# Performance work log

Hardware: AMD Instinct MI355X
Metric: run time of the kernel (lower is better)

Reference implementation:

```python
import jax, jax.numpy as jnp
import numpy as np
from jax import lax

HEADS, DIM_HEAD, LANDMARKS, PINV_ITERS = 8, 64, 256, 6
D = 512


def layernorm(x, w, b, eps=1e-5):
    mu = x.mean(-1, keepdims=True)
    var = ((x - mu) ** 2).mean(-1, keepdims=True)
    return (x - mu) * lax.rsqrt(var + eps) * w + b


def pinv_iter(x, iters=PINV_ITERS):
    # Moore-Penrose pseudo-inverse via Newton-Schulz (lucidrains nystrom-attention)
    abs_x = jnp.abs(x)
    z = jnp.swapaxes(x, -1, -2) / (jnp.max(abs_x.sum(-1)) * jnp.max(abs_x.sum(-2)))
    I = jnp.eye(x.shape[-1], dtype=x.dtype)
    for _ in range(iters):
        xz = x @ z
        z = 0.25 * z @ (13 * I - xz @ (15 * I - xz @ (7 * I - xz)))
    return z


def nystrom_attention(x, qkv_w, out_w, out_b, res_w):
    b, n, _ = x.shape
    m = LANDMARKS
    pad = (m - n % m) % m
    xp = jnp.pad(x, ((0, 0), (pad, 0), (0, 0)))  # left-pad seq to multiple of m
    n_p = n + pad
    q, k, v = jnp.split(xp @ qkv_w, 3, axis=-1)
    split = lambda t: t.reshape(b, n_p, HEADS, DIM_HEAD).transpose(0, 2, 1, 3)
    q, k, v = split(q), split(k), split(v)  # (b, h, n_p, d)
    q = q * DIM_HEAD ** -0.5
    l = n_p // m  # tokens per landmark
    q_l = q.reshape(b, HEADS, m, l, DIM_HEAD).mean(3)  # (b, h, m, d)
    k_l = k.reshape(b, HEADS, m, l, DIM_HEAD).mean(3)
    a1 = jax.nn.softmax(jnp.einsum('bhnd,bhmd->bhnm', q, k_l), -1)  # (b,h,n_p,m)
    a2 = jax.nn.softmax(jnp.einsum('bhmd,bhld->bhml', q_l, k_l), -1)  # (b,h,m,m)
    a3 = jax.nn.softmax(jnp.einsum('bhmd,bhnd->bhmn', q_l, k), -1)  # (b,h,m,n_p)
    out = (a1 @ pinv_iter(a2)) @ (a3 @ v)  # (b,h,n_p,d)
    # depthwise residual conv over the seq dim, kernel (33,1), one per head
    res = lax.conv_general_dilated(v, res_w, (1, 1), [(16, 16), (0, 0)],
                                   dimension_numbers=('NCHW', 'OIHW', 'NCHW'),
                                   feature_group_count=HEADS)
    out = out + res
    out = out.transpose(0, 2, 1, 3).reshape(b, n_p, HEADS * DIM_HEAD)
    return (out @ out_w + out_b)[:, -n:]


def ppeg(x, Hh, Ww, w7, b7, w5, b5, w3, b3):
    B, _, C = x.shape
    cls_tok, feat = x[:, :1], x[:, 1:]
    f = feat.transpose(0, 2, 1).reshape(B, C, Hh, Ww)
    def dwconv(w, bb, p):
        return lax.conv_general_dilated(f, w, (1, 1), [(p, p), (p, p)],
                                        dimension_numbers=('NCHW', 'OIHW', 'NCHW'),
                                        feature_group_count=C) + bb[None, :, None, None]
    y = f + dwconv(w7, b7, 3) + dwconv(w5, b5, 2) + dwconv(w3, b3, 1)
    y = y.reshape(B, C, Hh * Ww).transpose(0, 2, 1)
    return jnp.concatenate([cls_tok, y], axis=1)


def setup_inputs() -> dict:
    key = jax.random.key(0)
    ks = jax.random.split(key, 16)
    E, NC, H = 1024, 4, HEADS
    f32 = jnp.float32
    rn = lambda k, shp, s=0.02: (jax.random.normal(k, shp, f32) * s)
    return {
        'x': jax.random.normal(ks[0], (1, 40960, E), f32),
        'fc1_w': rn(ks[1], (E, D)), 'fc1_b': jnp.zeros((D,), f32),
        'cls_token': jax.random.normal(ks[2], (1, 1, D), f32),
        'l1_norm_w': jnp.ones((D,), f32), 'l1_norm_b': jnp.zeros((D,), f32),
        'l1_qkv_w': rn(ks[3], (D, 3 * D)),
        'l1_out_w': rn(ks[4], (D, D)), 'l1_out_b': jnp.zeros((D,), f32),
        'l1_res_w': rn(ks[5], (H, 1, 33, 1), 0.1),
        'ppeg_w7': rn(ks[6], (D, 1, 7, 7), 0.1), 'ppeg_b7': jnp.zeros((D,), f32),
        'ppeg_w5': rn(ks[7], (D, 1, 5, 5), 0.1), 'ppeg_b5': jnp.zeros((D,), f32),
        'ppeg_w3': rn(ks[8], (D, 1, 3, 3), 0.1), 'ppeg_b3': jnp.zeros((D,), f32),
        'l2_norm_w': jnp.ones((D,), f32), 'l2_norm_b': jnp.zeros((D,), f32),
        'l2_qkv_w': rn(ks[9], (D, 3 * D)),
        'l2_out_w': rn(ks[10], (D, D)), 'l2_out_b': jnp.zeros((D,), f32),
        'l2_res_w': rn(ks[11], (H, 1, 33, 1), 0.1),
        'norm_w': jnp.ones((D,), f32), 'norm_b': jnp.zeros((D,), f32),
        'fc3_w': rn(ks[12], (D, NC)), 'fc3_b': jnp.zeros((NC,), f32),
    }


def reference(x, fc1_w, fc1_b, cls_token, l1_norm_w, l1_norm_b, l1_qkv_w, l1_out_w, l1_out_b, l1_res_w, ppeg_w7, ppeg_b7, ppeg_w5, ppeg_b5, ppeg_w3, ppeg_b3, l2_norm_w, l2_norm_b, l2_qkv_w, l2_out_w, l2_out_b, l2_res_w, norm_w, norm_b, fc3_w, fc3_b):
    B, N, E = x.shape  # (1, 40960, 1024)
    POOL_OUT = 20480
    # AdaptiveMaxPool2d((20480, E)) on a (1, N, E) tensor: max-pool seq dim N -> 20480
    ft = x.reshape(B, POOL_OUT, N // POOL_OUT, E).max(axis=2)
    ft = jax.nn.relu(ft @ fc1_w + fc1_b)  # (1, 20480, 512)
    Hn = ft.shape[1]
    _H = int(np.ceil(np.sqrt(Hn)))  # 144
    add = _H * _H - Hn  # 256
    ft = jnp.concatenate([ft, ft[:, :add]], axis=1)  # (1, 20736, 512)
    h = jnp.concatenate([jnp.broadcast_to(cls_token, (B, 1, D)), ft], axis=1)  # 20737 tokens
    h = h + nystrom_attention(layernorm(h, l1_norm_w, l1_norm_b), l1_qkv_w, l1_out_w, l1_out_b, l1_res_w)
    h = ppeg(h, _H, _H, ppeg_w7, ppeg_b7, ppeg_w5, ppeg_b5, ppeg_w3, ppeg_b3)
    h = h + nystrom_attention(layernorm(h, l2_norm_w, l2_norm_b), l2_qkv_w, l2_out_w, l2_out_b, l2_res_w)
    h = layernorm(h, norm_w, norm_b)[:, 0]
    logits = h @ fc3_w + fc3_b
    return logits, jax.nn.softmax(logits, -1), jnp.argmax(logits, -1)
```

## Files before the change

### kernel.cpp

```cpp
#include <hip/hip_runtime.h>


constexpr int D_    = 512;
constexpr int E_    = 1024;
constexpr int NTOK  = 20737;
constexpr int NP_   = 20992;
constexpr int NH_   = 8;
constexpr int HD_   = 64;
constexpr int MLM   = 256;
constexpr int LCH   = 82;
constexpr int HHW   = 144;
constexpr int NFEAT = 20736;
constexpr int PADR  = 255;
constexpr int NCH   = 41;
constexpr int CHTOK = 512;

typedef __attribute__((ext_vector_type(8))) short bf16x8;
typedef __attribute__((ext_vector_type(4))) float f32x4;

__device__ __forceinline__ unsigned short f2bf(float f){
  unsigned int u = __float_as_uint(f);
  unsigned int r = u + 0x7fffu + ((u >> 16) & 1u);
  return (unsigned short)(r >> 16);
}
__device__ __forceinline__ float bfu(unsigned short u){
  return __uint_as_float((unsigned int)u << 16);
}

__device__ __forceinline__ float waveMaxF(float v){
#pragma unroll
  for (int o = 32; o > 0; o >>= 1) v = fmaxf(v, __shfl_xor(v, o));
  return v;
}
__device__ __forceinline__ float waveSumF(float v){
#pragma unroll
  for (int o = 32; o > 0; o >>= 1) v += __shfl_xor(v, o);
  return v;
}
__device__ __forceinline__ float blockMax256(float v, float* sbuf){
  v = waveMaxF(v);
  if ((threadIdx.x & 63) == 0) sbuf[threadIdx.x >> 6] = v;
  __syncthreads();
  float r = fmaxf(fmaxf(sbuf[0], sbuf[1]), fmaxf(sbuf[2], sbuf[3]));
  __syncthreads();
  return r;
}
__device__ __forceinline__ float blockSum256(float v, float* sbuf){
  v = waveSumF(v);
  if ((threadIdx.x & 63) == 0) sbuf[threadIdx.x >> 6] = v;
  __syncthreads();
  float r = sbuf[0] + sbuf[1] + sbuf[2] + sbuf[3];
  __syncthreads();
  return r;
}

__global__ __launch_bounds__(256) void wtrans_kernel(
    const float* __restrict__ W, unsigned short* __restrict__ Wt, int K, int N){
  __shared__ float tile[32][33];
  const int kb = blockIdx.x * 32, nb = blockIdx.y * 32;
  const int tx = threadIdx.x, ty = threadIdx.y;
  for (int i = ty; i < 32; i += 8) tile[i][tx] = W[(size_t)(kb + i) * N + nb + tx];
  __syncthreads();
  for (int i = ty; i < 32; i += 8)
    Wt[(size_t)(nb + i) * K + kb + tx] = f2bf(tile[tx][i]);
}

__global__ __launch_bounds__(256) void pool_bf16_kernel(
    const float* __restrict__ x, unsigned short* __restrict__ Ah){
  size_t idx4 = ((size_t)blockIdx.x * 256 + threadIdx.x) * 4;
  size_t m = idx4 >> 10, e = idx4 & 1023;
  float4 a = *(const float4*)(x + (m * 2) * E_ + e);
  float4 b = *(const float4*)(x + (m * 2 + 1) * E_ + e);
  unsigned long long pk =
      (unsigned long long)f2bf(fmaxf(a.x, b.x))
    | ((unsigned long long)f2bf(fmaxf(a.y, b.y)) << 16)
    | ((unsigned long long)f2bf(fmaxf(a.z, b.z)) << 32)
    | ((unsigned long long)f2bf(fmaxf(a.w, b.w)) << 48);
  *(unsigned long long*)(Ah + idx4) = pk;
}

__device__ __forceinline__ void mfma_tile64(
    const unsigned short* __restrict__ A, int arows, int bm,
    const unsigned short* __restrict__ Bt, int bn, int K,
    f32x4 acc[2][2], unsigned short* As, unsigned short* Bs){
  const int t = threadIdx.x;
  const int lane = t & 63, wave = t >> 6;
  const int wr = wave >> 1, wc = wave & 1;
  const int m16 = lane & 15, quad = lane >> 4;
  for (int kc = 0; kc < K; kc += 64){
    for (int idx = t; idx < 512; idx += 256){
      int row = idx >> 3, off = (idx & 7) * 8;
      int ga = bm + row;
      ulonglong2 av = {0ull, 0ull};
      if (ga < arows) av = *(const ulonglong2*)(A + (size_t)ga * K + kc + off);
      *(ulonglong2*)(As + row * 72 + off) = av;
      ulonglong2 bv = *(const ulonglong2*)(Bt + (size_t)(bn + row) * K + kc + off);
      *(ulonglong2*)(Bs + row * 72 + off) = bv;
    }
    __syncthreads();
#pragma unroll
    for (int k2 = 0; k2 < 64; k2 += 32){
      bf16x8 a0 = *(const bf16x8*)(As + (wr * 32 + m16) * 72 + k2 + quad * 8);
      bf16x8 a1 = *(const bf16x8*)(As + (wr * 32 + 16 + m16) * 72 + k2 + quad * 8);
      bf16x8 b0 = *(const bf16x8*)(Bs + (wc * 32 + m16) * 72 + k2 + quad * 8);
      bf16x8 b1 = *(const bf16x8*)(Bs + (wc * 32 + 16 + m16) * 72 + k2 + quad * 8);
      acc[0][0] = __builtin_amdgcn_mfma_f32_16x16x32_bf16(a0, b0, acc[0][0], 0, 0, 0);
      acc[0][1] = __builtin_amdgcn_mfma_f32_16x16x32_bf16(a0, b1, acc[0][1], 0, 0, 0);
      acc[1][0] = __builtin_amdgcn_mfma_f32_16x16x32_bf16(a1, b0, acc[1][0], 0, 0, 0);
      acc[1][1] = __builtin_amdgcn_mfma_f32_16x16x32_bf16(a1, b1, acc[1][1], 0, 0, 0);
    }
    __syncthreads();
  }
}

__global__ __launch_bounds__(256) void fc1_mfma_kernel(
    const unsigned short* __restrict__ Ah, const unsigned short* __restrict__ Bt,
    const float* __restrict__ bias, float* __restrict__ h){
  __shared__ unsigned short As[64 * 72], Bs[64 * 72];
  f32x4 z4 = {0.f, 0.f, 0.f, 0.f};
  f32x4 acc[2][2] = {{z4, z4}, {z4, z4}};
  const int bm = blockIdx.x * 64, bn = blockIdx.y * 64;
  mfma_tile64(Ah, 20480, bm, Bt, bn, E_, acc, As, Bs);
  const int lane = threadIdx.x & 63, wave = threadIdx.x >> 6;
  const int wr = wave >> 1, wc = wave & 1;
  const int m16 = lane & 15, quad = lane >> 4;
#pragma unroll
  for (int mi = 0; mi < 2; mi++)
#pragma unroll
    for (int ni = 0; ni < 2; ni++){
      int col = bn + wc * 32 + ni * 16 + m16;
      float bv = bias[col];
#pragma unroll
      for (int r = 0; r < 4; r++){
        int row = bm + wr * 32 + mi * 16 + quad * 4 + r;
        float vv = fmaxf(acc[mi][ni][r] + bv, 0.f);
        h[(size_t)(1 + row) * D_ + col] = vv;
        if (row < 256) h[(size_t)(20481 + row) * D_ + col] = vv;
      }
    }
}

__global__ void cls_kernel(const float* __restrict__ cls, float* __restrict__ h){
  int c = blockIdx.x * 256 + threadIdx.x;
  if (c < D_) h[c] = cls[c];
}

__global__ __launch_bounds__(256) void ln_pad_kernel(
    const float* __restrict__ h, const float* __restrict__ w,
    const float* __restrict__ b, unsigned short* __restrict__ xph){
  const int r = blockIdx.x;
  const int t = threadIdx.x;
  if (r < PADR){
    xph[(size_t)r * D_ + t] = 0;
    xph[(size_t)r * D_ + 256 + t] = 0;
    return;
  }
  __shared__ float s4[4];
  const float* x = h + (size_t)(r - PADR) * D_;
  float a0 = x[t], a1 = x[t + 256];
  float mu = blockSum256(a0 + a1, s4) * (1.f / 512.f);
  float d0 = a0 - mu, d1 = a1 - mu;
  float var = blockSum256(d0 * d0 + d1 * d1, s4) * (1.f / 512.f);
  float rs = rsqrtf(var + 1e-5f);
  xph[(size_t)r * D_ + t]       = f2bf(d0 * rs * w[t] + b[t]);
  xph[(size_t)r * D_ + 256 + t] = f2bf(d1 * rs * w[t + 256] + b[t + 256]);
}

__global__ __launch_bounds__(256) void qkv_mfma_kernel(
    const unsigned short* __restrict__ A, const unsigned short* __restrict__ Bt,
    unsigned short* __restrict__ q16, unsigned short* __restrict__ k16,
    unsigned short* __restrict__ v16){
  __shared__ unsigned short As[64 * 72], Bs[64 * 72];
  f32x4 z4 = {0.f, 0.f, 0.f, 0.f};
  f32x4 acc[2][2] = {{z4, z4}, {z4, z4}};
  const int bm = blockIdx.x * 64, bn = blockIdx.y * 64;
  mfma_tile64(A, NP_, bm, Bt, bn, D_, acc, As, Bs);
  const int lane = threadIdx.x & 63, wave = threadIdx.x >> 6;
  const int wr = wave >> 1, wc = wave & 1;
  const int m16 = lane & 15, quad = lane >> 4;
#pragma unroll
  for (int mi = 0; mi < 2; mi++)
#pragma unroll
    for (int ni = 0; ni < 2; ni++){
      int col = bn + wc * 32 + ni * 16 + m16;
      int which = col >> 9, hh = (col >> 6) & 7, d = col & 63;
      size_t cbase = (size_t)hh * NP_ * HD_ + d;
      unsigned short* dst;
      float sc = 1.f;
      if (which == 0){ dst = q16; sc = 0.125f; }
      else if (which == 1) dst = k16;
      else dst = v16;
#pragma unroll
      for (int r = 0; r < 4; r++){
        int row = bm + wr * 32 + mi * 16 + quad * 4 + r;
        dst[cbase + (size_t)row * HD_] = f2bf(acc[mi][ni][r] * sc);
      }
    }
}

__global__ __launch_bounds__(64) void landmark_kernel(
    const unsigned short* __restrict__ q16, const unsigned short* __restrict__ k16,
    float* __restrict__ ql, float* __restrict__ kl,
    unsigned short* __restrict__ qlh, unsigned short* __restrict__ klh){
  const int im = blockIdx.x, h = blockIdx.y, d = threadIdx.x;
  size_t base = ((size_t)h * NP_ + (size_t)im * LCH) * HD_ + d;
  float sq = 0.f, sk = 0.f;
  for (int r = 0; r < LCH; r++){
    sq += bfu(q16[base + (size_t)r * HD_]);
    sk += bfu(k16[base + (size_t)r * HD_]);
  }
  float qm = sq * (1.f / 82.f), km = sk * (1.f / 82.f);
  size_t oidx = ((size_t)h * MLM + im) * HD_ + d;
  ql[oidx] = qm;  qlh[oidx] = f2bf(qm);
  kl[oidx] = km;  klh[oidx] = f2bf(km);
}

__global__ __launch_bounds__(256) void a2_kernel(
    const float* __restrict__ ql, const float* __restrict__ kl,
    float* __restrict__ a2){
  const int im = blockIdx.x, h = blockIdx.y, t = threadIdx.x;
  __shared__ __align__(16) float qs[64];
  __shared__ float s4[4];
  if (t < 64) qs[t] = ql[((size_t)h * MLM + im) * HD_ + t];
  __syncthreads();
  const float4* kr4 = (const float4*)(kl + ((size_t)h * MLM + t) * HD_);
  const float4* qs4 = (const float4*)qs;
  float s = 0.f;
#pragma unroll
  for (int d4 = 0; d4 < 16; d4++){
    float4 kv = kr4[d4], qv = qs4[d4];
    s += qv.x*kv.x + qv.y*kv.y + qv.z*kv.z + qv.w*kv.w;
  }
  float mx = blockMax256(s, s4);
  float e = __expf(s - mx);
  float S = blockSum256(e, s4);
  a2[((size_t)h * MLM + im) * MLM + t] = e / S;
}

__global__ __launch_bounds__(256) void pinv_scale_kernel(
    const float* __restrict__ a2, float* __restrict__ scal){
  const int h = blockIdx.x, j = threadIdx.x;
  const float* A = a2 + (size_t)h * MLM * MLM;
  float rs = 0.f, cs = 0.f;
  for (int t = 0; t < MLM; t++){
    rs += fabsf(A[(size_t)j * MLM + t]);
    cs += fabsf(A[(size_t)t * MLM + j]);
  }
  __shared__ float s4[4];
  float rmax = blockMax256(rs, s4);
  float cmax = blockMax256(cs, s4);
  if (j == 0){ scal[h * 2] = rmax; scal[h * 2 + 1] = cmax; }
}

__global__ __launch_bounds__(256) void pinv_init_kernel(
    const float* __restrict__ a2, const float* __restrict__ scal,
    float* __restrict__ z){
  const int i = blockIdx.x, h = blockIdx.y, j = threadIdx.x;
  float rmax = scal[0], cmax = scal[1];
#pragma unroll
  for (int hh = 1; hh < 8; hh++){
    rmax = fmaxf(rmax, scal[hh * 2]);
    cmax = fmaxf(cmax, scal[hh * 2 + 1]);
  }
  float inv = 1.f / (rmax * cmax);
  z[((size_t)h * MLM + i) * MLM + j] = a2[((size_t)h * MLM + j) * MLM + i] * inv;
}

__global__ __launch_bounds__(256) void bmm256_mfma_kernel(
    const float* __restrict__ Ab, const float* __restrict__ Bb,
    float* __restrict__ Cb, float c0, float sgn, float c1){
  __shared__ unsigned short Ash[64 * 40], Asl[64 * 40];
  __shared__ unsigned short Bsh[64 * 40], Bsl[64 * 40];
  const int h = blockIdx.z;
  const float* A = Ab + (size_t)h * 65536;
  const float* B = Bb + (size_t)h * 65536;
  float* C = Cb + (size_t)h * 65536;
  const int bm = blockIdx.x * 64, bn = blockIdx.y * 64;
  const int t = threadIdx.x, lane = t & 63, w = t >> 6;
  const int wr = w >> 1, wc = w & 1, m16 = lane & 15, quad = lane >> 4;
  f32x4 z4 = {0.f, 0.f, 0.f, 0.f};
  f32x4 acc[2][2] = {{z4, z4}, {z4, z4}};
  for (int kc = 0; kc < 256; kc += 32){
    {
      int row = t >> 2, c8 = (t & 3) * 8;
      const float* src = A + (size_t)(bm + row) * 256 + kc + c8;
      float xs[8];
      *(float4*)(xs)     = *(const float4*)src;
      *(float4*)(xs + 4) = *(const float4*)(src + 4);
#pragma unroll
      for (int j = 0; j < 8; j++){
        unsigned short hi = f2bf(xs[j]);
        Ash[row * 40 + c8 + j] = hi;
        Asl[row * 40 + c8 + j] = f2bf(xs[j] - bfu(hi));
      }
      int k = t >> 3, n8 = (t & 7) * 8;
      const float* bsrc = B + (size_t)(kc + k) * 256 + bn + n8;
      float ys[8];
      *(float4*)(ys)     = *(const float4*)bsrc;
      *(float4*)(ys + 4) = *(const float4*)(bsrc + 4);
#pragma unroll
      for (int j = 0; j < 8; j++){
        float xv = sgn * ys[j];
        if (kc + k == bn + n8 + j) xv += c0;
        unsigned short hi = f2bf(xv);
        Bsh[(n8 + j) * 40 + k] = hi;
        Bsl[(n8 + j) * 40 + k] = f2bf(xv - bfu(hi));
      }
    }
    __syncthreads();
    bf16x8 ah[2], al[2], bh[2], bl[2];
#pragma unroll
    for (int mi = 0; mi < 2; mi++){
      ah[mi] = *(const bf16x8*)(Ash + (wr * 32 + mi * 16 + m16) * 40 + quad * 8);
      al[mi] = *(const bf16x8*)(Asl + (wr * 32 + mi * 16 + m16) * 40 + quad * 8);
      bh[mi] = *(const bf16x8*)(Bsh + (wc * 32 + mi * 16 + m16) * 40 + quad * 8);
      bl[mi] = *(const bf16x8*)(Bsl + (wc * 32 + mi * 16 + m16) * 40 + quad * 8);
    }
#pragma unroll
    for (int mi = 0; mi < 2; mi++)
#pragma unroll
      for (int ni = 0; ni < 2; ni++){
        acc[mi][ni] = __builtin_amdgcn_mfma_f32_16x16x32_bf16(ah[mi], bh[ni], acc[mi][ni], 0, 0, 0);
        acc[mi][ni] = __builtin_amdgcn_mfma_f32_16x16x32_bf16(ah[mi], bl[ni], acc[mi][ni], 0, 0, 0);
        acc[mi][ni] = __builtin_amdgcn_mfma_f32_16x16x32_bf16(al[mi], bh[ni], acc[mi][ni], 0, 0, 0);
      }
    __syncthreads();
  }
#pragma unroll
  for (int mi = 0; mi < 2; mi++)
#pragma unroll
    for (int ni = 0; ni < 2; ni++)
#pragma unroll
      for (int r = 0; r < 4; r++){
        int row = bm + wr * 32 + mi * 16 + quad * 4 + r;
        int col = bn + wc * 32 + ni * 16 + m16;
        C[(size_t)row * 256 + col] = c1 * acc[mi][ni][r];
      }
}

__global__ __launch_bounds__(256) void a3v_part_kernel(
    const unsigned short* __restrict__ qlh, const unsigned short* __restrict__ k16,
    const unsigned short* __restrict__ v16, float* __restrict__ pacc,
    float* __restrict__ pml){
  __shared__ __align__(16) unsigned short qs16[64 * 72];
  __shared__ __align__(16) unsigned short kb16[64 * 72];
  __shared__ __align__(16) unsigned short vt16[64 * 72];
  const int lt = blockIdx.x, h = blockIdx.y, ch = blockIdx.z;
  const int t = threadIdx.x;
  const int lane = t & 63, w = t >> 6;
  const int m16 = lane & 15, quad = lane >> 4;

  const unsigned short* qg = qlh + ((size_t)h * MLM + lt * 64) * HD_;
  for (int idx = t; idx < 512; idx += 256){
    int row = idx >> 3, off = (idx & 7) * 8;
    *(uint4*)(qs16 + row * 72 + off) = *(const uint4*)(qg + (size_t)row * HD_ + off);
  }
  f32x4 z4 = {0.f, 0.f, 0.f, 0.f};
  f32x4 acc_o[4] = {z4, z4, z4, z4};
  float mreg[4], lreg[4];
#pragma unroll
  for (int r = 0; r < 4; r++){ mreg[r] = -3.0e38f; lreg[r] = 0.f; }
  const unsigned short* kg = k16 + ((size_t)h * NP_ + ch * CHTOK) * HD_;
  const unsigned short* vg = v16 + ((size_t)h * NP_ + ch * CHTOK) * HD_;

  for (int sc = 0; sc < 8; sc++){
    __syncthreads();
    for (int idx = t; idx < 512; idx += 256){
      int row = idx >> 3, off = (idx & 7) * 8;
      *(uint4*)(kb16 + row * 72 + off) =
          *(const uint4*)(kg + (size_t)(sc * 64 + row) * HD_ + off);
      uint4 pv = *(const uint4*)(vg + (size_t)(sc * 64 + row) * HD_ + off);
      unsigned int uu[4] = {pv.x, pv.y, pv.z, pv.w};
#pragma unroll
      for (int j = 0; j < 4; j++){
        vt16[(off + 2 * j)     * 72 + row] = (unsigned short)(uu[j] & 0xffffu);
        vt16[(off + 2 * j + 1) * 72 + row] = (unsigned short)(uu[j] >> 16);
      }
    }
    __syncthreads();
    f32x4 acc_s[4] = {z4, z4, z4, z4};
#pragma unroll
    for (int kc = 0; kc < 64; kc += 32){
      bf16x8 a = *(const bf16x8*)(qs16 + (w * 16 + m16) * 72 + kc + quad * 8);
#pragma unroll
      for (int ni = 0; ni < 4; ni++){
        bf16x8 b = *(const bf16x8*)(kb16 + (ni * 16 + m16) * 72 + kc + quad * 8);
        acc_s[ni] = __builtin_amdgcn_mfma_f32_16x16x32_bf16(a, b, acc_s[ni], 0, 0, 0);
      }
    }
    __syncthreads();
#pragma unroll
    for (int r = 0; r < 4; r++){
      float cm = fmaxf(fmaxf(acc_s[0][r], acc_s[1][r]), fmaxf(acc_s[2][r], acc_s[3][r]));
#pragma unroll
      for (int o = 1; o < 16; o <<= 1) cm = fmaxf(cm, __shfl_xor(cm, o));
      float mn = fmaxf(mreg[r], cm);
      float scl = __expf(mreg[r] - mn);
      float p0 = __expf(acc_s[0][r] - mn), p1 = __expf(acc_s[1][r] - mn);
      float p2 = __expf(acc_s[2][r] - mn), p3 = __expf(acc_s[3][r] - mn);
      float ls = (p0 + p1) + (p2 + p3);
#pragma unroll
      for (int o = 1; o < 16; o <<= 1) ls += __shfl_xor(ls, o);
      lreg[r] = lreg[r] * scl + ls;
      mreg[r] = mn;
      acc_o[0][r] *= scl; acc_o[1][r] *= scl;
      acc_o[2][r] *= scl; acc_o[3][r] *= scl;
      int prow = (w * 16 + quad * 4 + r) * 72 + m16;
      kb16[prow + 0]  = f2bf(p0);
      kb16[prow + 16] = f2bf(p1);
      kb16[prow + 32] = f2bf(p2);
      kb16[prow + 48] = f2bf(p3);
    }
    __syncthreads();
#pragma unroll
    for (int kc = 0; kc < 64; kc += 32){
      bf16x8 a = *(const bf16x8*)(kb16 + (w * 16 + m16) * 72 + kc + quad * 8);
#pragma unroll
      for (int ni = 0; ni < 4; ni++){
        bf16x8 b = *(const bf16x8*)(vt16 + (ni * 16 + m16) * 72 + kc + quad * 8);
        acc_o[ni] = __builtin_amdgcn_mfma_f32_16x16x32_bf16(a, b, acc_o[ni], 0, 0, 0);
      }
    }
  }
#pragma unroll
  for (int r = 0; r < 4; r++){
    int im = lt * 64 + w * 16 + quad * 4 + r;
    size_t base = ((size_t)h * NCH + ch) * MLM + im;
#pragma unroll
    for (int ni = 0; ni < 4; ni++)
      pacc[base * HD_ + ni * 16 + m16] = acc_o[ni][r];
    if (m16 == 0){
      pml[base * 2]     = mreg[r];
      pml[base * 2 + 1] = lreg[r];
    }
  }
}

__global__ __launch_bounds__(64) void a3v_combine_kernel(
    const float* __restrict__ pacc, const float* __restrict__ pml,
    float* __restrict__ t1){
  const int im = blockIdx.x, h = blockIdx.y, lane = threadIdx.x;
  float M = -3.0e38f;
  for (int c = 0; c < NCH; c++)
    M = fmaxf(M, pml[(((size_t)h * NCH + c) * MLM + im) * 2]);
  float accv = 0.f, L = 0.f;
  for (int c = 0; c < NCH; c++){
    size_t base = ((size_t)h * NCH + c) * MLM + im;
    float mc = pml[base * 2], lc = pml[base * 2 + 1];
    float w = __expf(mc - M);
    accv += w * pacc[base * HD_ + lane];
    L += w * lc;
  }
  t1[((size_t)h * MLM + im) * HD_ + lane] = accv / L;
}

__global__ __launch_bounds__(256) void zt1_kernel(
    const float* __restrict__ z, const float* __restrict__ t1,
    unsigned short* __restrict__ t2t){
  const int h = blockIdx.y;
  const int t = threadIdx.x;
  const int d = t & 63, ri = t >> 6;
  const int im = blockIdx.x * 4 + ri;
  const float* zr = z + ((size_t)h * MLM + im) * MLM;
  const float* t1h = t1 + (size_t)h * MLM * HD_;
  float acc = 0.f;
#pragma unroll 8
  for (int kk = 0; kk < MLM; kk++) acc += zr[kk] * t1h[(size_t)kk * HD_ + d];
  t2t[((size_t)h * HD_ + d) * MLM + im] = f2bf(acc);
}

__global__ __launch_bounds__(256) void out_tile_kernel(
    const unsigned short* __restrict__ q16, const unsigned short* __restrict__ klh,
    const unsigned short* __restrict__ t2t, const unsigned short* __restrict__ v16,
    const float* __restrict__ resw, unsigned short* __restrict__ outh){
  __shared__ __align__(16) unsigned short smem[64 * 72 * 2 + 64 * 264];
  unsigned short* qs16 = smem;
  unsigned short* kb16 = smem + 64 * 72;
  unsigned short* Ps   = smem + 64 * 72 * 2;
  const int tile = blockIdx.x, h = blockIdx.y;
  const int n0 = PADR + tile * 64;
  const int t = threadIdx.x;
  const int lane = t & 63, w = t >> 6;
  const int m16 = lane & 15, quad = lane >> 4;

  {
    const unsigned short* qh = q16 + (size_t)h * NP_ * HD_;
    for (int idx = t; idx < 512; idx += 256){
      int row = idx >> 3, off = (idx & 7) * 8;
      int n = n0 + row;
      uint4 val = {0u, 0u, 0u, 0u};
      if (n < NP_) val = *(const uint4*)(qh + (size_t)n * HD_ + off);
      *(uint4*)(qs16 + row * 72 + off) = val;
    }
  }
  f32x4 z4 = {0.f, 0.f, 0.f, 0.f};
  f32x4 acc_s[16];
#pragma unroll
  for (int i = 0; i < 16; i++) acc_s[i] = z4;
  const unsigned short* klg = klh + (size_t)h * MLM * HD_;
  for (int m = 0; m < 4; m++){
    __syncthreads();
    for (int idx = t; idx < 512; idx += 256){
      int row = idx >> 3, off = (idx & 7) * 8;
      *(uint4*)(kb16 + row * 72 + off) =
          *(const uint4*)(klg + (size_t)(m * 64 + row) * HD_ + off);
    }
    __syncthreads();
#pragma unroll
    for (int kc = 0; kc < 64; kc += 32){
      bf16x8 a = *(const bf16x8*)(qs16 + (w * 16 + m16) * 72 + kc + quad * 8);
#pragma unroll
      for (int ni = 0; ni < 4; ni++){
        bf16x8 b = *(const bf16x8*)(kb16 + (ni * 16 + m16) * 72 + kc + quad * 8);
        acc_s[m * 4 + ni] = __builtin_amdgcn_mfma_f32_16x16x32_bf16(a, b, acc_s[m * 4 + ni], 0, 0, 0);
      }
    }
  }
  __syncthreads();
#pragma unroll
  for (int r = 0; r < 4; r++){
    float mx = acc_s[0][r];
#pragma unroll
    for (int mc = 1; mc < 16; mc++) mx = fmaxf(mx, acc_s[mc][r]);
#pragma unroll
    for (int o = 1; o < 16; o <<= 1) mx = fmaxf(mx, __shfl_xor(mx, o));
    float p[16]; float sum = 0.f;
#pragma unroll
    for (int mc = 0; mc < 16; mc++){ p[mc] = __expf(acc_s[mc][r] - mx); sum += p[mc]; }
#pragma unroll
    for (int o = 1; o < 16; o <<= 1) sum += __shfl_xor(sum, o);
    float inv = 1.f / sum;
    int prow = (w * 16 + quad * 4 + r) * 264;
#pragma unroll
    for (int mc = 0; mc < 16; mc++)
      Ps[prow + (mc >> 2) * 64 + (mc & 3) * 16 + m16] = f2bf(p[mc] * inv);
  }
  f32x4 acc_o[4] = {z4, z4, z4, z4};
  const unsigned short* t2g = t2t + (size_t)h * HD_ * MLM;
  for (int ch = 0; ch < 4; ch++){
    __syncthreads();
    {
      int row = t >> 2, c8 = (t & 3) * 16;
      const unsigned short* src = t2g + (size_t)row * MLM + ch * 64 + c8;
      *(uint4*)(kb16 + row * 72 + c8)     = *(const uint4*)src;
      *(uint4*)(kb16 + row * 72 + c8 + 8) = *(const uint4*)(src + 8);
    }
    __syncthreads();
#pragma unroll
    for (int kc = 0; kc < 64; kc += 32){
      bf16x8 a = *(const bf16x8*)(Ps + (w * 16 + m16) * 264 + ch * 64 + kc + quad * 8);
#pragma unroll
      for (int ni = 0; ni < 4; ni++){
        bf16x8 b = *(const bf16x8*)(kb16 + (ni * 16 + m16) * 72 + kc + quad * 8);
        acc_o[ni] = __builtin_amdgcn_mfma_f32_16x16x32_bf16(a, b, acc_o[ni], 0, 0, 0);
      }
    }
  }
  __syncthreads();
  float* Obuf = (float*)Ps;
  unsigned short* vtile = (unsigned short*)(Obuf + 64 * 66);
#pragma unroll
  for (int r = 0; r < 4; r++){
    int row = w * 16 + quad * 4 + r;
#pragma unroll
    for (int ni = 0; ni < 4; ni++)
      Obuf[row * 66 + ni * 16 + m16] = acc_o[ni][r];
  }
  {
    const unsigned short* vh = v16 + (size_t)h * NP_ * HD_;
    for (int idx = t; idx < 768; idx += 256){
      int row = idx >> 3, off = (idx & 7) * 8;
      int nn = n0 - 16 + row;
      uint4 val = {0u, 0u, 0u, 0u};
      if (nn < NP_) val = *(const uint4*)(vh + (size_t)nn * HD_ + off);
      *(uint4*)(vtile + row * 72 + off) = val;
    }
  }
  __syncthreads();
  float wreg[33];
  {
    const float* wr = resw + h * 33;
#pragma unroll
    for (int kk = 0; kk < 33; kk++) wreg[kk] = wr[kk];
  }
  const int ty = t >> 4, tx = t & 15;
#pragma unroll
  for (int i = 0; i < 4; i++){
    int lrow = ty * 4 + i;
    float c0v = 0.f, c1v = 0.f, c2v = 0.f, c3v = 0.f;
    for (int kk = 0; kk < 33; kk++){
      uint2 uv = *(const uint2*)(vtile + (lrow + kk) * 72 + tx * 4);
      float wv = wreg[kk];
      c0v += __uint_as_float(uv.x << 16) * wv;
      c1v += __uint_as_float(uv.x & 0xffff0000u) * wv;
      c2v += __uint_as_float(uv.y << 16) * wv;
      c3v += __uint_as_float(uv.y & 0xffff0000u) * wv;
    }
    int trow = tile * 64 + lrow;
    if (trow < NTOK){
      const float* orow = Obuf + lrow * 66 + tx * 4;
      unsigned long long pk =
          (unsigned long long)f2bf(orow[0] + c0v)
        | ((unsigned long long)f2bf(orow[1] + c1v) << 16)
        | ((unsigned long long)f2bf(orow[2] + c2v) << 32)
        | ((unsigned long long)f2bf(orow[3] + c3v) << 48);
      *(unsigned long long*)(outh + (size_t)trow * D_ + h * HD_ + tx * 4) = pk;
    }
  }
}

__global__ __launch_bounds__(256) void proj_mfma_kernel(
    const unsigned short* __restrict__ A, const unsigned short* __restrict__ Bt,
    const float* __restrict__ bias, float* __restrict__ h){
  __shared__ unsigned short As[64 * 72], Bs[64 * 72];
  f32x4 z4 = {0.f, 0.f, 0.f, 0.f};
  f32x4 acc[2][2] = {{z4, z4}, {z4, z4}};
  const int bm = blockIdx.x * 64, bn = blockIdx.y * 64;
  mfma_tile64(A, NTOK, bm, Bt, bn, D_, acc, As, Bs);
  const int lane = threadIdx.x & 63, wave = threadIdx.x >> 6;
  const int wr = wave >> 1, wc = wave & 1;
  const int m16 = lane & 15, quad = lane >> 4;
#pragma unroll
  for (int mi = 0; mi < 2; mi++)
#pragma unroll
    for (int ni = 0; ni < 2; ni++){
      int col = bn + wc * 32 + ni * 16 + m16;
      float bv = bias[col];
#pragma unroll
      for (int r = 0; r < 4; r++){
        int row = bm + wr * 32 + mi * 16 + quad * 4 + r;
        if (row < NTOK) h[(size_t)row * D_ + col] += acc[mi][ni][r] + bv;
      }
    }
}

__global__ __launch_bounds__(512) void ppeg_combine_kernel(
    const float* __restrict__ w7, const float* __restrict__ b7,
    const float* __restrict__ w5, const float* __restrict__ b5,
    const float* __restrict__ w3, const float* __restrict__ b3,
    float* __restrict__ wcomb, float* __restrict__ bcomb){
  const int c = threadIdx.x;
#pragma unroll
  for (int i = 0; i < 7; i++){
#pragma unroll
    for (int j = 0; j < 7; j++){
      int di = i - 3, dj = j - 3;
      float wv = w7[(size_t)c * 49 + i * 7 + j];
      if (di >= -2 && di <= 2 && dj >= -2 && dj <= 2)
        wv += w5[(size_t)c * 25 + (di + 2) * 5 + (dj + 2)];
      if (di >= -1 && di <= 1 && dj >= -1 && dj <= 1)
        wv += w3[(size_t)c * 9 + (di + 1) * 3 + (dj + 1)];
      if (di == 0 && dj == 0) wv += 1.f;
      wcomb[(size_t)(i * 7 + j) * 512 + c] = wv;
    }
  }
  bcomb[c] = b7[c] + b5[c] + b3[c];
}

__global__ __launch_bounds__(512) void ppeg_conv_kernel(
    const float* __restrict__ h, const float* __restrict__ wcomb,
    const float* __restrict__ bcomb, float* __restrict__ tmp){
  const int c = threadIdx.x;
  const int y = blockIdx.y;
  const int x0 = blockIdx.x * 8;
  float wc[49];
#pragma unroll
  for (int kk = 0; kk < 49; kk++) wc[kk] = wcomb[(size_t)kk * 512 + c];
  float acc[8];
  const float bv = bcomb[c];
#pragma unroll
  for (int p = 0; p < 8; p++) acc[p] = bv;
#pragma unroll
  for (int i = 0; i < 7; i++){
    const int yy = y + i - 3;
    if (yy < 0 || yy >= HHW) continue;
    const float* hrow = h + (size_t)(1 + yy * HHW) * D_ + c;
    float line[14];
#pragma unroll
    for (int j = 0; j < 14; j++){
      const int xx = x0 + j - 3;
      line[j] = (xx >= 0 && xx < HHW) ? hrow[(size_t)xx * D_] : 0.f;
    }
#pragma unroll
    for (int p = 0; p < 8; p++)
#pragma unroll
      for (int j = 0; j < 7; j++)
        acc[p] += line[p + j] * wc[i * 7 + j];
  }
#pragma unroll
  for (int p = 0; p < 8; p++)
    tmp[(size_t)(y * HHW + x0 + p) * D_ + c] = acc[p];
}

__global__ void ppeg_copy_kernel(const float* __restrict__ tmp, float* __restrict__ h){
  size_t idx = (size_t)blockIdx.x * 256 + threadIdx.x;
  if (idx < (size_t)NFEAT * D_) h[idx + D_] = tmp[idx];
}

__global__ __launch_bounds__(512) void final_kernel(
    const float* __restrict__ h, const float* __restrict__ w,
    const float* __restrict__ b, const float* __restrict__ fc3w,
    const float* __restrict__ fc3b, float* __restrict__ out){
  __shared__ float vec[512];
  __shared__ float s8[8];
  __shared__ float lg[4];
  const int t = threadIdx.x;
  float x = h[t];
  float v = waveSumF(x);
  if ((t & 63) == 0) s8[t >> 6] = v;
  __syncthreads();
  float sum = 0.f;
#pragma unroll
  for (int i = 0; i < 8; i++) sum += s8[i];
  float mu = sum * (1.f / 512.f);
  __syncthreads();
  float d = x - mu;
  v = waveSumF(d * d);
  if ((t & 63) == 0) s8[t >> 6] = v;
  __syncthreads();
  float var = 0.f;
#pragma unroll
  for (int i = 0; i < 8; i++) var += s8[i];
  var *= (1.f / 512.f);
  float rs = rsqrtf(var + 1e-5f);
  vec[t] = d * rs * w[t] + b[t];
  __syncthreads();
  if (t < 4){
    float acc = fc3b[t];
    for (int kk = 0; kk < 512; kk++) acc += vec[kk] * fc3w[kk * 4 + t];
    lg[t] = acc;
  }
  __syncthreads();
  if (t == 0){
    float m = fmaxf(fmaxf(lg[0], lg[1]), fmaxf(lg[2], lg[3]));
    float e[4], se = 0.f;
#pragma unroll
    for (int i = 0; i < 4; i++){ e[i] = __expf(lg[i] - m); se += e[i]; }
    int am = 0; float bm = lg[0];
#pragma unroll
    for (int i = 1; i < 4; i++) if (lg[i] > bm){ bm = lg[i]; am = i; }
#pragma unroll
    for (int i = 0; i < 4; i++){ out[i] = lg[i]; out[4 + i] = e[i] / se; }
    out[8] = (float)am;
  }
}

extern "C" void kernel_launch(void* const* d_in, const int* in_sizes, int n_in,
                              void* d_out, int out_size, void* d_ws, size_t ws_size,
                              hipStream_t stream) {
  const float* x       = (const float*)d_in[0];
  const float* fc1_w   = (const float*)d_in[1];
  const float* fc1_b   = (const float*)d_in[2];
  const float* cls_tok = (const float*)d_in[3];
  const float* l1_nw   = (const float*)d_in[4];
  const float* l1_nb   = (const float*)d_in[5];
  const float* l1_qkvw = (const float*)d_in[6];
  const float* l1_outw = (const float*)d_in[7];
  const float* l1_outb = (const float*)d_in[8];
  const float* l1_resw = (const float*)d_in[9];
  const float* ppeg_w7 = (const float*)d_in[10];
  const float* ppeg_b7 = (const float*)d_in[11];
  const float* ppeg_w5 = (const float*)d_in[12];
  const float* ppeg_b5 = (const float*)d_in[13];
  const float* ppeg_w3 = (const float*)d_in[14];
  const float* ppeg_b3 = (const float*)d_in[15];
  const float* l2_nw   = (const float*)d_in[16];
  const float* l2_nb   = (const float*)d_in[17];
  const float* l2_qkvw = (const float*)d_in[18];
  const float* l2_outw = (const float*)d_in[19];
  const float* l2_outb = (const float*)d_in[20];
  const float* l2_resw = (const float*)d_in[21];
  const float* norm_w  = (const float*)d_in[22];
  const float* norm_b  = (const float*)d_in[23];
  const float* fc3_w   = (const float*)d_in[24];
  const float* fc3_b   = (const float*)d_in[25];

  float* W = (float*)d_ws;
  size_t o = 0;
  float* hbuf = W + o; o += (size_t)NTOK * D_;
  float* xp   = W + o; o += (size_t)NP_ * D_;
  float* qb   = W + o; o += (size_t)NH_ * NP_ * HD_;
  float* kb   = W + o; o += (size_t)NH_ * NP_ * HD_;
  float* vb   = W + o; o += (size_t)NH_ * NP_ * HD_;
  float* qlb  = W + o; o += (size_t)NH_ * MLM * HD_;
  float* klb  = W + o; o += (size_t)NH_ * MLM * HD_;
  float* a2b  = W + o; o += (size_t)NH_ * MLM * MLM;
  float* z0   = W + o; o += (size_t)NH_ * MLM * MLM;
  float* z1   = W + o; o += (size_t)NH_ * MLM * MLM;
  float* ta   = W + o; o += (size_t)NH_ * MLM * MLM;
  float* tb   = W + o; o += (size_t)NH_ * MLM * MLM;
  float* tc   = W + o; o += (size_t)NH_ * MLM * MLM;
  float* t1b  = W + o; o += (size_t)NH_ * MLM * HD_;
  float* t2r  = W + o; o += (size_t)NH_ * MLM * HD_;
  float* scalf = W + o; o += 16;
  float* wcomb = W + o; o += 49 * 512;
  float* bcomb = W + o; o += 512;
  unsigned short* fc1_wt  = (unsigned short*)(W + o); o += (size_t)D_ * E_ / 2;
  unsigned short* qkv_wt1 = (unsigned short*)(W + o); o += (size_t)1536 * D_ / 2;
  unsigned short* qkv_wt2 = (unsigned short*)(W + o); o += (size_t)1536 * D_ / 2;
  unsigned short* out_wt1 = (unsigned short*)(W + o); o += (size_t)D_ * D_ / 2;
  unsigned short* out_wt2 = (unsigned short*)(W + o); o += (size_t)D_ * D_ / 2;
  unsigned short* qlh = (unsigned short*)(W + o); o += (size_t)NH_ * MLM * HD_ / 2;
  unsigned short* klh = (unsigned short*)(W + o); o += (size_t)NH_ * MLM * HD_ / 2;

  unsigned short* xph = (unsigned short*)xp;
  float* pacc = xp;
  float* pml  = xp + (size_t)NH_ * NCH * MLM * HD_;
  unsigned short* outh = (unsigned short*)xp;
  unsigned short* Ah  = (unsigned short*)qb;
  unsigned short* q16 = (unsigned short*)qb;
  unsigned short* k16 = (unsigned short*)kb;
  unsigned short* v16 = (unsigned short*)vb;
  unsigned short* t2t = (unsigned short*)t2r;

  wtrans_kernel<<<dim3(E_ / 32, D_ / 32), dim3(32, 8), 0, stream>>>(fc1_w, fc1_wt, E_, D_);
  wtrans_kernel<<<dim3(D_ / 32, 1536 / 32), dim3(32, 8), 0, stream>>>(l1_qkvw, qkv_wt1, D_, 1536);
  wtrans_kernel<<<dim3(D_ / 32, 1536 / 32), dim3(32, 8), 0, stream>>>(l2_qkvw, qkv_wt2, D_, 1536);
  wtrans_kernel<<<dim3(D_ / 32, D_ / 32), dim3(32, 8), 0, stream>>>(l1_outw, out_wt1, D_, D_);
  wtrans_kernel<<<dim3(D_ / 32, D_ / 32), dim3(32, 8), 0, stream>>>(l2_outw, out_wt2, D_, D_);
  ppeg_combine_kernel<<<1, 512, 0, stream>>>(ppeg_w7, ppeg_b7, ppeg_w5, ppeg_b5,
                                             ppeg_w3, ppeg_b3, wcomb, bcomb);

  pool_bf16_kernel<<<20480, 256, 0, stream>>>(x, Ah);
  fc1_mfma_kernel<<<dim3(320, 8), 256, 0, stream>>>(Ah, fc1_wt, fc1_b, hbuf);
  cls_kernel<<<2, 256, 0, stream>>>(cls_tok, hbuf);

  auto run_layer = [&](const float* nw, const float* nb,
                       const unsigned short* qkvwt, const unsigned short* outwt,
                       const float* outb, const float* resw){
    ln_pad_kernel<<<NP_, 256, 0, stream>>>(hbuf, nw, nb, xph);
    qkv_mfma_kernel<<<dim3(328, 24), 256, 0, stream>>>(xph, qkvwt, q16, k16, v16);
    landmark_kernel<<<dim3(256, 8), 64, 0, stream>>>(q16, k16, qlb, klb, qlh, klh);
    a2_kernel<<<dim3(256, 8), 256, 0, stream>>>(qlb, klb, a2b);
    pinv_scale_kernel<<<8, 256, 0, stream>>>(a2b, scalf);
    pinv_init_kernel<<<dim3(256, 8), 256, 0, stream>>>(a2b, scalf, z0);
    float* zc = z0; float* za = z1;
    for (int it = 0; it < 6; it++){
      bmm256_mfma_kernel<<<dim3(4, 4, 8), 256, 0, stream>>>(a2b, zc, ta, 0.f, 1.f, 1.f);
      bmm256_mfma_kernel<<<dim3(4, 4, 8), 256, 0, stream>>>(ta, ta, tb, 7.f, -1.f, 1.f);
      bmm256_mfma_kernel<<<dim3(4, 4, 8), 256, 0, stream>>>(ta, tb, tc, 15.f, -1.f, 1.f);
      bmm256_mfma_kernel<<<dim3(4, 4, 8), 256, 0, stream>>>(zc, tc, za, 13.f, -1.f, 0.25f);
      float* tswap = zc; zc = za; za = tswap;
    }
    a3v_part_kernel<<<dim3(4, 8, NCH), 256, 0, stream>>>(qlh, k16, v16, pacc, pml);
    a3v_combine_kernel<<<dim3(256, 8), 64, 0, stream>>>(pacc, pml, t1b);
    zt1_kernel<<<dim3(64, 8), 256, 0, stream>>>(zc, t1b, t2t);
    out_tile_kernel<<<dim3(325, 8), 256, 0, stream>>>(q16, klh, t2t, v16, resw, outh);
    proj_mfma_kernel<<<dim3(325, 8), 256, 0, stream>>>(outh, outwt, outb, hbuf);
  };

  run_layer(l1_nw, l1_nb, qkv_wt1, out_wt1, l1_outb, l1_resw);
  ppeg_conv_kernel<<<dim3(HHW / 8, HHW), 512, 0, stream>>>(hbuf, wcomb, bcomb, xp);
  ppeg_copy_kernel<<<(NFEAT * D_ + 255) / 256, 256, 0, stream>>>(xp, hbuf);
  run_layer(l2_nw, l2_nb, qkv_wt2, out_wt2, l2_outb, l2_resw);
  final_kernel<<<1, 512, 0, stream>>>(hbuf, norm_w, norm_b, fc3_w, fc3_b, (float*)d_out);
}
```

Measured before the change: 1.703 ms.

## Enlarge MFMA GEMM tiles to 128x128 and drop PPEG copy via second buffer

The shared MFMA GEMM helper now computes 128x128 output tiles, with each wave owning a 64x64 block of 4x4 MFMA accumulators. fc1, qkv and proj grids shrink to match, raising arithmetic intensity per LDS load and cutting global reloads of A and B. The PPEG conv now writes directly into a second hidden-state buffer, and only row 0 is copied, replacing the full-tensor copy kernel. The costs are higher register and LDS usage per block, which may lower occupancy, and fewer blocks in flight for the smaller GEMMs.

```diff
diff --git a/kernel.cpp b/kernel.cpp
--- a/kernel.cpp
+++ b/kernel.cpp
@@ -79,16 +79,16 @@
   *(unsigned long long*)(Ah + idx4) = pk;
 }
 
-__device__ __forceinline__ void mfma_tile64(
+__device__ __forceinline__ void mfma_tile128(
     const unsigned short* __restrict__ A, int arows, int bm,
     const unsigned short* __restrict__ Bt, int bn, int K,
-    f32x4 acc[2][2], unsigned short* As, unsigned short* Bs){
+    f32x4 acc[4][4], unsigned short* As, unsigned short* Bs){
   const int t = threadIdx.x;
   const int lane = t & 63, wave = t >> 6;
   const int wr = wave >> 1, wc = wave & 1;
   const int m16 = lane & 15, quad = lane >> 4;
   for (int kc = 0; kc < K; kc += 64){
-    for (int idx = t; idx < 512; idx += 256){
+    for (int idx = t; idx < 1024; idx += 256){
       int row = idx >> 3, off = (idx & 7) * 8;
       int ga = bm + row;
       ulonglong2 av = {0ull, 0ull};
@@ -100,14 +100,18 @@
     __syncthreads();
 #pragma unroll
     for (int k2 = 0; k2 < 64; k2 += 32){
-      bf16x8 a0 = *(const bf16x8*)(As + (wr * 32 + m16) * 72 + k2 + quad * 8);
-      bf16x8 a1 = *(const bf16x8*)(As + (wr * 32 + 16 + m16) * 72 + k2 + quad * 8);
-      bf16x8 b0 = *(const bf16x8*)(Bs + (wc * 32 + m16) * 72 + k2 + quad * 8);
-      bf16x8 b1 = *(const bf16x8*)(Bs + (wc * 32 + 16 + m16) * 72 + k2 + quad * 8);
-      acc[0][0] = __builtin_amdgcn_mfma_f32_16x16x32_bf16(a0, b0, acc[0][0], 0, 0, 0);
-      acc[0][1] = __builtin_amdgcn_mfma_f32_16x16x32_bf16(a0, b1, acc[0][1], 0, 0, 0);
-      acc[1][0] = __builtin_amdgcn_mfma_f32_16x16x32_bf16(a1, b0, acc[1][0], 0, 0, 0);
-      acc[1][1] = __builtin_amdgcn_mfma_f32_16x16x32_bf16(a1, b1, acc[1][1], 0, 0, 0);
+      bf16x8 af[4], bf[4];
+#pragma unroll
+      for (int mi = 0; mi < 4; mi++)
+        af[mi] = *(const bf16x8*)(As + (wr * 64 + mi * 16 + m16) * 72 + k2 + quad * 8);
+#pragma unroll
+      for (int ni = 0; ni < 4; ni++)
+        bf[ni] = *(const bf16x8*)(Bs + (wc * 64 + ni * 16 + m16) * 72 + k2 + quad * 8);
+#pragma unroll
+      for (int mi = 0; mi < 4; mi++)
+#pragma unroll
+        for (int ni = 0; ni < 4; ni++)
+          acc[mi][ni] = __builtin_amdgcn_mfma_f32_16x16x32_bf16(af[mi], bf[ni], acc[mi][ni], 0, 0, 0);
     }
     __syncthreads();
   }
@@ -116,23 +120,27 @@
 __global__ __launch_bounds__(256) void fc1_mfma_kernel(
     const unsigned short* __restrict__ Ah, const unsigned short* __restrict__ Bt,
     const float* __restrict__ bias, float* __restrict__ h){
-  __shared__ unsigned short As[64 * 72], Bs[64 * 72];
+  __shared__ unsigned short As[128 * 72], Bs[128 * 72];
   f32x4 z4 = {0.f, 0.f, 0.f, 0.f};
-  f32x4 acc[2][2] = {{z4, z4}, {z4, z4}};
-  const int bm = blockIdx.x * 64, bn = blockIdx.y * 64;
-  mfma_tile64(Ah, 20480, bm, Bt, bn, E_, acc, As, Bs);
+  f32x4 acc[4][4];
+#pragma unroll
+  for (int i = 0; i < 4; i++)
+#pragma unroll
+    for (int j = 0; j < 4; j++) acc[i][j] = z4;
+  const int bm = blockIdx.x * 128, bn = blockIdx.y * 128;
+  mfma_tile128(Ah, 20480, bm, Bt, bn, E_, acc, As, Bs);
   const int lane = threadIdx.x & 63, wave = threadIdx.x >> 6;
   const int wr = wave >> 1, wc = wave & 1;
   const int m16 = lane & 15, quad = lane >> 4;
 #pragma unroll
-  for (int mi = 0; mi < 2; mi++)
-#pragma unroll
-    for (int ni = 0; ni < 2; ni++){
-      int col = bn + wc * 32 + ni * 16 + m16;
+  for (int mi = 0; mi < 4; mi++)
+#pragma unroll
+    for (int ni = 0; ni < 4; ni++){
+      int col = bn + wc * 64 + ni * 16 + m16;
       float bv = bias[col];
 #pragma unroll
       for (int r = 0; r < 4; r++){
-        int row = bm + wr * 32 + mi * 16 + quad * 4 + r;
+        int row = bm + wr * 64 + mi * 16 + quad * 4 + r;
         float vv = fmaxf(acc[mi][ni][r] + bv, 0.f);
         h[(size_t)(1 + row) * D_ + col] = vv;
         if (row < 256) h[(size_t)(20481 + row) * D_ + col] = vv;
@@ -143,6 +151,11 @@
 __global__ void cls_kernel(const float* __restrict__ cls, float* __restrict__ h){
   int c = blockIdx.x * 256 + threadIdx.x;
   if (c < D_) h[c] = cls[c];
+}
+
+__global__ void row0_copy_kernel(const float* __restrict__ src, float* __restrict__ dst){
+  int c = blockIdx.x * 256 + threadIdx.x;
+  if (c < D_) dst[c] = src[c];
 }
 
 __global__ __launch_bounds__(256) void ln_pad_kernel(
@@ -170,19 +183,23 @@
     const unsigned short* __restrict__ A, const unsigned short* __restrict__ Bt,
     unsigned short* __restrict__ q16, unsigned short* __restrict__ k16,
     unsigned short* __restrict__ v16){
-  __shared__ unsigned short As[64 * 72], Bs[64 * 72];
+  __shared__ unsigned short As[128 * 72], Bs[128 * 72];
   f32x4 z4 = {0.f, 0.f, 0.f, 0.f};
-  f32x4 acc[2][2] = {{z4, z4}, {z4, z4}};
-  const int bm = blockIdx.x * 64, bn = blockIdx.y * 64;
-  mfma_tile64(A, NP_, bm, Bt, bn, D_, acc, As, Bs);
+  f32x4 acc[4][4];
+#pragma unroll
+  for (int i = 0; i < 4; i++)
+#pragma unroll
+    for (int j = 0; j < 4; j++) acc[i][j] = z4;
+  const int bm = blockIdx.x * 128, bn = blockIdx.y * 128;
+  mfma_tile128(A, NP_, bm, Bt, bn, D_, acc, As, Bs);
   const int lane = threadIdx.x & 63, wave = threadIdx.x >> 6;
   const int wr = wave >> 1, wc = wave & 1;
   const int m16 = lane & 15, quad = lane >> 4;
 #pragma unroll
-  for (int mi = 0; mi < 2; mi++)
-#pragma unroll
-    for (int ni = 0; ni < 2; ni++){
-      int col = bn + wc * 32 + ni * 16 + m16;
+  for (int mi = 0; mi < 4; mi++)
+#pragma unroll
+    for (int ni = 0; ni < 4; ni++){
+      int col = bn + wc * 64 + ni * 16 + m16;
       int which = col >> 9, hh = (col >> 6) & 7, d = col & 63;
       size_t cbase = (size_t)hh * NP_ * HD_ + d;
       unsigned short* dst;
@@ -192,7 +209,7 @@
       else dst = v16;
 #pragma unroll
       for (int r = 0; r < 4; r++){
-        int row = bm + wr * 32 + mi * 16 + quad * 4 + r;
+        int row = bm + wr * 64 + mi * 16 + quad * 4 + r;
         dst[cbase + (size_t)row * HD_] = f2bf(acc[mi][ni][r] * sc);
       }
     }
@@ -612,23 +629,27 @@
 __global__ __launch_bounds__(256) void proj_mfma_kernel(
     const unsigned short* __restrict__ A, const unsigned short* __restrict__ Bt,
     const float* __restrict__ bias, float* __restrict__ h){
-  __shared__ unsigned short As[64 * 72], Bs[64 * 72];
+  __shared__ unsigned short As[128 * 72], Bs[128 * 72];
   f32x4 z4 = {0.f, 0.f, 0.f, 0.f};
-  f32x4 acc[2][2] = {{z4, z4}, {z4, z4}};
-  const int bm = blockIdx.x * 64, bn = blockIdx.y * 64;
-  mfma_tile64(A, NTOK, bm, Bt, bn, D_, acc, As, Bs);
+  f32x4 acc[4][4];
+#pragma unroll
+  for (int i = 0; i < 4; i++)
+#pragma unroll
+    for (int j = 0; j < 4; j++) acc[i][j] = z4;
+  const int bm = blockIdx.x * 128, bn = blockIdx.y * 128;
+  mfma_tile128(A, NTOK, bm, Bt, bn, D_, acc, As, Bs);
   const int lane = threadIdx.x & 63, wave = threadIdx.x >> 6;
   const int wr = wave >> 1, wc = wave & 1;
   const int m16 = lane & 15, quad = lane >> 4;
 #pragma unroll
-  for (int mi = 0; mi < 2; mi++)
-#pragma unroll
-    for (int ni = 0; ni < 2; ni++){
-      int col = bn + wc * 32 + ni * 16 + m16;
+  for (int mi = 0; mi < 4; mi++)
+#pragma unroll
+    for (int ni = 0; ni < 4; ni++){
+      int col = bn + wc * 64 + ni * 16 + m16;
       float bv = bias[col];
 #pragma unroll
       for (int r = 0; r < 4; r++){
-        int row = bm + wr * 32 + mi * 16 + quad * 4 + r;
+        int row = bm + wr * 64 + mi * 16 + quad * 4 + r;
         if (row < NTOK) h[(size_t)row * D_ + col] += acc[mi][ni][r] + bv;
       }
     }
@@ -659,7 +680,7 @@
 
 __global__ __launch_bounds__(512) void ppeg_conv_kernel(
     const float* __restrict__ h, const float* __restrict__ wcomb,
-    const float* __restrict__ bcomb, float* __restrict__ tmp){
+    const float* __restrict__ bcomb, float* __restrict__ h2){
   const int c = threadIdx.x;
   const int y = blockIdx.y;
   const int x0 = blockIdx.x * 8;
@@ -689,12 +710,7 @@
   }
 #pragma unroll
   for (int p = 0; p < 8; p++)
-    tmp[(size_t)(y * HHW + x0 + p) * D_ + c] = acc[p];
-}
-
-__global__ void ppeg_copy_kernel(const float* __restrict__ tmp, float* __restrict__ h){
-  size_t idx = (size_t)blockIdx.x * 256 + threadIdx.x;
-  if (idx < (size_t)NFEAT * D_) h[idx + D_] = tmp[idx];
+    h2[(size_t)(1 + y * HHW + x0 + p) * D_ + c] = acc[p];
 }
 
 __global__ __launch_bounds__(512) void final_kernel(
@@ -802,6 +818,7 @@
   unsigned short* out_wt2 = (unsigned short*)(W + o); o += (size_t)D_ * D_ / 2;
   unsigned short* qlh = (unsigned short*)(W + o); o += (size_t)NH_ * MLM * HD_ / 2;
   unsigned short* klh = (unsigned short*)(W + o); o += (size_t)NH_ * MLM * HD_ / 2;
+  float* hbuf2 = W + o; o += (size_t)NTOK * D_;
 
   unsigned short* xph = (unsigned short*)xp;
   float* pacc = xp;
@@ -822,14 +839,14 @@
                                              ppeg_w3, ppeg_b3, wcomb, bcomb);
 
   pool_bf16_kernel<<<20480, 256, 0, stream>>>(x, Ah);
-  fc1_mfma_kernel<<<dim3(320, 8), 256, 0, stream>>>(Ah, fc1_wt, fc1_b, hbuf);
+  fc1_mfma_kernel<<<dim3(160, 4), 256, 0, stream>>>(Ah, fc1_wt, fc1_b, hbuf);
   cls_kernel<<<2, 256, 0, stream>>>(cls_tok, hbuf);
 
-  auto run_layer = [&](const float* nw, const float* nb,
+  auto run_layer = [&](float* hcur, const float* nw, const float* nb,
                        const unsigned short* qkvwt, const unsigned short* outwt,
                        const float* outb, const float* resw){
-    ln_pad_kernel<<<NP_, 256, 0, stream>>>(hbuf, nw, nb, xph);
-    qkv_mfma_kernel<<<dim3(328, 24), 256, 0, stream>>>(xph, qkvwt, q16, k16, v16);
+    ln_pad_kernel<<<NP_, 256, 0, stream>>>(hcur, nw, nb, xph);
+    qkv_mfma_kernel<<<dim3(164, 12), 256, 0, stream>>>(xph, qkvwt, q16, k16, v16);
     landmark_kernel<<<dim3(256, 8), 64, 0, stream>>>(q16, k16, qlb, klb, qlh, klh);
     a2_kernel<<<dim3(256, 8), 256, 0, stream>>>(qlb, klb, a2b);
     pinv_scale_kernel<<<8, 256, 0, stream>>>(a2b, scalf);
@@ -846,12 +863,12 @@
     a3v_combine_kernel<<<dim3(256, 8), 64, 0, stream>>>(pacc, pml, t1b);
     zt1_kernel<<<dim3(64, 8), 256, 0, stream>>>(zc, t1b, t2t);
     out_tile_kernel<<<dim3(325, 8), 256, 0, stream>>>(q16, klh, t2t, v16, resw, outh);
-    proj_mfma_kernel<<<dim3(325, 8), 256, 0, stream>>>(outh, outwt, outb, hbuf);
+    proj_mfma_kernel<<<dim3(163, 4), 256, 0, stream>>>(outh, outwt, outb, hcur);
   };
 
-  run_layer(l1_nw, l1_nb, qkv_wt1, out_wt1, l1_outb, l1_resw);
-  ppeg_conv_kernel<<<dim3(HHW / 8, HHW), 512, 0, stream>>>(hbuf, wcomb, bcomb, xp);
-  ppeg_copy_kernel<<<(NFEAT * D_ + 255) / 256, 256, 0, stream>>>(xp, hbuf);
-  run_layer(l2_nw, l2_nb, qkv_wt2, out_wt2, l2_outb, l2_resw);
-  final_kernel<<<1, 512, 0, stream>>>(hbuf, norm_w, norm_b, fc3_w, fc3_b, (float*)d_out);
-}
+  run_layer(hbuf, l1_nw, l1_nb, qkv_wt1, out_wt1, l1_outb, l1_resw);
+  ppeg_conv_kernel<<<dim3(HHW / 8, HHW), 512, 0, stream>>>(hbuf, wcomb, bcomb, hbuf2);
+  row0_copy_kernel<<<2, 256, 0, stream>>>(hbuf, hbuf2);
+  run_layer(hbuf2, l2_nw, l2_nb, qkv_wt2, out_wt2, l2_outb, l2_resw);
+  final_kernel<<<1, 512, 0, stream>>>(hbuf2, norm_w, norm_b, fc3_w, fc3_b, (float*)d_out);
+}
```

Result: no change. 1.700 ms (-0.2%).
